# Optimization experiments

Measured on AMD Instinct MI355X. Metric: run time of the kernel, lower is better.

## Reference

```python
import jax, jax.numpy as jnp
import numpy as np

OFF_THRESH = 0.5  # specials.OFF_THRESH
INF = 1e10        # specials.INF


def _neighbor_gather(v):
    # v: [B, C, 3, 3, K, Hp, Wp] -> [B, C, 9, K, Hp, Wp]
    # entry (s,t) at output pixel (h,w) reads cell (s,t) of source pixel
    # (h-(s-1), w-(t-1)), i.e. the pixel whose window cell points at (h,w).
    B, C, _, _, K, Hp, Wp = v.shape
    vp = jnp.pad(v, ((0, 0), (0, 0), (0, 0), (0, 0), (0, 0), (1, 1), (1, 1)))
    slabs = [vp[:, :, s, t, :, 2 - s:2 - s + Hp, 2 - t:2 - t + Wp]
             for s in range(3) for t in range(3)]
    return jnp.stack(slabs, axis=2)


def _rays(cam_inv, Hp, Wp):
    # normalized (x/z, y/z) camera rays for padded pixel grid extended by 1
    xs = jnp.arange(-1, Wp + 1, dtype=jnp.float32)
    ys = jnp.arange(-1, Hp + 1, dtype=jnp.float32)
    u, v = jnp.meshgrid(xs, ys)                      # [Hp+2, Wp+2]
    hom = jnp.stack([u, v, jnp.ones_like(u)], 0)     # [3, Hp+2, Wp+2]
    r = jnp.einsum('ij,jhw->ihw', cam_inv, hom)
    return r[:2] / r[2:3]                            # [2, Hp+2, Wp+2]


def _smap_forward(x, cam):
    B = x.shape[0]
    H, W = x.shape[-2], x.shape[-1]
    Hp, Wp = H + 2, W + 2
    # add_pad: zero-pad spatially by 1 (3x3 window)
    xp = jnp.pad(x, ((0, 0), (0, 0), (1, 1), (1, 1)))
    xv, yv, zv, rm = xp[:, None, 0], xp[:, None, 1], xp[:, None, 2], xp[:, None, 3]  # [B,1,Hp,Wp]

    # ---- SMap3x3.forward ----
    cam_inv = jnp.linalg.inv(cam)
    rays = _rays(cam_inv, Hp, Wp)
    zs = jnp.where(zv > 0.0, zv, 1.0)
    px, py = xv / zs, yv / zs                        # projected normalized coords
    costs = []
    for s in range(3):
        for t in range(3):
            rx = rays[0, s:s + Hp, t:t + Wp]
            ry = rays[1, s:s + Hp, t:t + Wp]
            costs.append((px - rx) ** 2 + (py - ry) ** 2)
    key_query = jnp.stack(costs, axis=2)             # [B,1,9,Hp,Wp]

    idx = jnp.argmin(key_query, axis=2)              # argmax(-kq)
    weights_b = jax.nn.one_hot(idx, 9, axis=2, dtype=x.dtype)   # [B,1,9,Hp,Wp]
    valid = (rm > OFF_THRESH) & (zv > 0.0)           # [B,1,Hp,Wp]
    weights_b = jnp.where(valid[:, :, None], weights_b, 0.0)
    temp = jax.nn.one_hot(jnp.full((1,), 4), 9, dtype=x.dtype).reshape(1, 1, 9, 1, 1)
    bad = (rm > OFF_THRESH) & ~(zv > 0.0)
    weights_b = jnp.where(bad[:, :, None], temp, weights_b)

    xyz = jnp.stack([xv, yv, zv], axis=2)            # [B,1,3,Hp,Wp]
    wdet = jax.lax.stop_gradient(weights_b).reshape(B, 1, 3, 3, Hp, Wp)
    new_xyz = jnp.einsum('bcsthw,bczhw->bcstzhw', wdet, xyz)  # [B,1,3,3,3,Hp,Wp]
    weights_b2 = jnp.where(valid[:, :, None], weights_b, temp)
    new_rm = (jax.lax.stop_gradient(weights_b2) * rm[:, :, None]).reshape(B, 1, 3, 3, 1, Hp, Wp)
    nxz = jnp.concatenate([new_xyz, new_rm], axis=4)  # [B,1,3,3,4,Hp,Wp]

    # ---- calculate_weights ----
    zch = jax.lax.stop_gradient(nxz[:, :, :, :, 2:3])           # detached z channel
    gz = _neighbor_gather(zch)                                  # [B,1,9,1,Hp,Wp]
    gz = jnp.where(gz > 0.0, gz, INF)                           # agg(..., factor=INF)
    val = jnp.min(gz, axis=2, keepdims=True)
    sidx = jnp.argmin(gz, axis=2, keepdims=True)
    sidx = jnp.where((val > 0.0) & (val < INF), sidx, 4)
    sel = jax.nn.one_hot(sidx[:, :, 0], 9, axis=2, dtype=x.dtype)  # [B,1,9,1,Hp,Wp]
    gall = _neighbor_gather(nxz)                                # [B,1,9,4,Hp,Wp]
    out = jnp.sum(gall * sel, axis=2)                           # [B,1,4,Hp,Wp]
    # center crop back to original size
    out = out[:, :, :, 1:1 + H, 1:1 + W].reshape(B, 4, H, W)
    return out


def setup_inputs() -> dict:
    key = jax.random.key(0)
    k1, k2, k3 = jax.random.split(key, 3)
    B, H, W = 4, 512, 640
    xy = jax.random.normal(k1, (B, 2, H, W), dtype=jnp.float32)
    z = jax.random.uniform(k2, (B, 1, H, W), minval=0.5, maxval=5.0, dtype=jnp.float32)
    m = jax.random.uniform(k3, (B, 1, H, W), dtype=jnp.float32)
    x = jnp.concatenate([xy, z, m], axis=1)          # channels: x, y, z, mask
    cam = jnp.asarray(np.array([[500.0, 0.0, W / 2.0],
                                [0.0, 500.0, H / 2.0],
                                [0.0, 0.0, 1.0]], dtype=np.float32))
    return {"x": x, "cam": cam}


def reference(x, cam):
    return _smap_forward(x, cam)
```

## Files before the change

### kernel.cpp

```cpp
#include <hip/hip_runtime.h>

#define BT 32
#define HT (BT + 2)
#define PP (HT + 1)

__global__ __launch_bounds__(256) void smap_fused(
    const float* __restrict__ x, const float* __restrict__ cam,
    float* __restrict__ out, int B, int H, int W)
{
    __shared__ float2 szk[HT][PP];
    __shared__ float2 sxy[HT][PP];
    __shared__ float  srm[HT][PP];

    const int b  = blockIdx.z;
    const int h0 = blockIdx.y * BT;
    const int w0 = blockIdx.x * BT;
    const int tx = threadIdx.x;
    const int ty = threadIdx.y;
    const int tid = ty * 32 + tx;

    const float a00 = cam[0], a01 = cam[1], a02 = cam[2];
    const float a10 = cam[3], a11 = cam[4], a12 = cam[5];
    const float a20 = cam[6], a21 = cam[7], a22 = cam[8];
    const float m00 = a11 * a22 - a12 * a21;
    const float m01 = a10 * a22 - a12 * a20;
    const float m02 = a10 * a21 - a11 * a20;
    const float det = a00 * m00 - a01 * m01 + a02 * m02;
    const float i00 = m00 / det;
    const float i01 = (a02 * a21 - a01 * a22) / det;
    const float i02 = (a01 * a12 - a02 * a11) / det;
    const float i10 = (a12 * a20 - a10 * a22) / det;
    const float i11 = (a00 * a22 - a02 * a20) / det;
    const float i12 = (a02 * a10 - a00 * a12) / det;
    const float i20 = m02 / det;
    const float i21 = (a01 * a20 - a00 * a21) / det;
    const float i22 = (a00 * a11 - a01 * a10) / det;

    const bool fastcam = (i20 == 0.0f) && (i21 == 0.0f) && (i22 == 1.0f);
    const bool fastsep = fastcam &&
        (__float_as_uint(i01) == 0u) && (__float_as_uint(i10) == 0u);

    const size_t HW = (size_t)H * W;
    const float* xb = x + (size_t)b * 4 * HW;

    for (int item = tid; item < HT * HT; item += 256) {
        const int i = item / HT, j = item - i * HT;
        const int gh = h0 - 1 + i, gw = w0 - 1 + j;
        float xv = 0.f, yv = 0.f, zv = 0.f, rm = 0.f;
        if (gh >= 0 && gh < H && gw >= 0 && gw < W) {
            const size_t off = (size_t)gh * W + gw;
            xv = xb[off];
            yv = xb[HW + off];
            zv = xb[2 * HW + off];
            rm = xb[3 * HW + off];
        }
        const float zs = (zv > 0.f) ? zv : 1.0f;
        const float px = __fdiv_rn(xv, zs);
        const float py = __fdiv_rn(yv, zs);

        float best = __builtin_inff();
        int bi = 0;
        if (fastsep) {
            float f[3], g[3];
            #pragma unroll
            for (int t = 0; t < 3; ++t) {
                const float u  = (float)(gw + t);
                const float rx = __fadd_rn(__fmul_rn(i00, u), i02);
                const float dx = __fsub_rn(px, rx);
                f[t] = __fmul_rn(dx, dx);
            }
            #pragma unroll
            for (int s = 0; s < 3; ++s) {
                const float v  = (float)(gh + s);
                const float ry = __fadd_rn(__fmul_rn(i11, v), i12);
                const float dy = __fsub_rn(py, ry);
                g[s] = __fmul_rn(dy, dy);
            }
            #pragma unroll
            for (int n = 0; n < 9; ++n) {
                const float c = __fadd_rn(f[n % 3], g[n / 3]);
                if (c < best) { best = c; bi = n; }
            }
        } else {
            float A0[3], A1[3], B0[3], B1[3];
            #pragma unroll
            for (int t = 0; t < 3; ++t) {
                const float u = (float)(gw + t);
                A0[t] = __fmul_rn(i00, u);
                A1[t] = __fmul_rn(i10, u);
            }
            #pragma unroll
            for (int s = 0; s < 3; ++s) {
                const float v = (float)(gh + s);
                B0[s] = __fmul_rn(i01, v);
                B1[s] = __fmul_rn(i11, v);
            }
            #pragma unroll
            for (int n = 0; n < 9; ++n) {
                const int s = n / 3, t = n % 3;
                const float r0 = __fadd_rn(__fadd_rn(A0[t], B0[s]), i02);
                const float r1 = __fadd_rn(__fadd_rn(A1[t], B1[s]), i12);
                float rx, ry;
                if (fastcam) {
                    rx = r0; ry = r1;
                } else {
                    const float u = (float)(gw + t), v = (float)(gh + s);
                    const float r2 = __fadd_rn(__fadd_rn(__fmul_rn(i20, u), __fmul_rn(i21, v)), i22);
                    rx = __fdiv_rn(r0, r2);
                    ry = __fdiv_rn(r1, r2);
                }
                const float dx = __fsub_rn(px, rx);
                const float dy = __fsub_rn(py, ry);
                const float c  = __fadd_rn(__fmul_rn(dx, dx), __fmul_rn(dy, dy));
                if (c < best) { best = c; bi = n; }
            }
        }

        const bool validp = (rm > 0.5f) && (zv > 0.0f);
        const bool badp   = (rm > 0.5f) && !(zv > 0.0f);
        const int k = validp ? bi : (badp ? 4 : 9);
        szk[i][j] = make_float2(zv, __int_as_float(k));
        sxy[i][j] = make_float2(xv, yv);
        srm[i][j] = rm;
    }
    __syncthreads();

    const int rbase = 4 * ty;
    float2 rA[3], rB[3], rC[3];
    #pragma unroll
    for (int c = 0; c < 3; ++c) {
        rA[c] = szk[rbase][tx + c];
        rB[c] = szk[rbase + 1][tx + c];
    }

    #pragma unroll
    for (int q = 0; q < 4; ++q) {
        const int rq = rbase + q;
        #pragma unroll
        for (int c = 0; c < 3; ++c) rC[c] = szk[rq + 2][tx + c];

        float bz = 1e10f;
        int bli = rq + 1, blj = tx + 1;
        #pragma unroll
        for (int t = 0; t < 3; ++t) {
            const float z = rC[2 - t].x;
            const int   k = __float_as_int(rC[2 - t].y);
            const float cand = (k == t && z > 0.f) ? z : 1e10f;
            if (cand < bz) { bz = cand; bli = rq + 2; blj = tx + 2 - t; }
        }
        #pragma unroll
        for (int t = 0; t < 3; ++t) {
            const float z = rB[2 - t].x;
            const int   k = __float_as_int(rB[2 - t].y);
            const float cand = (k == 3 + t && z > 0.f) ? z : 1e10f;
            if (cand < bz) { bz = cand; bli = rq + 1; blj = tx + 2 - t; }
        }
        #pragma unroll
        for (int t = 0; t < 3; ++t) {
            const float z = rA[2 - t].x;
            const int   k = __float_as_int(rA[2 - t].y);
            const float cand = (k == 6 + t && z > 0.f) ? z : 1e10f;
            if (cand < bz) { bz = cand; bli = rq; blj = tx + 2 - t; }
        }
        const bool found = bz < 1e10f;

        const float2 vxy = sxy[bli][blj];
        const float  vrm = srm[bli][blj];

        float ox, oy, oz, orm;
        if (found) {
            ox = vxy.x; oy = vxy.y; oz = bz; orm = vrm;
        } else {
            const int   kc = __float_as_int(rB[1].y);
            const float zc = rB[1].x;
            const bool  k4 = (kc == 4);
            const bool  validp = (vrm > 0.5f) && (zc > 0.f);
            ox = k4 ? vxy.x : 0.f;
            oy = k4 ? vxy.y : 0.f;
            oz = k4 ? zc    : 0.f;
            orm = (k4 || !validp) ? vrm : 0.f;
        }

        const int h = h0 + rq, w = w0 + tx;
        const size_t obase = (size_t)b * 4 * HW + (size_t)h * W + w;
        __builtin_nontemporal_store(ox,  &out[obase]);
        __builtin_nontemporal_store(oy,  &out[obase + HW]);
        __builtin_nontemporal_store(oz,  &out[obase + 2 * HW]);
        __builtin_nontemporal_store(orm, &out[obase + 3 * HW]);

        #pragma unroll
        for (int c = 0; c < 3; ++c) { rA[c] = rB[c]; rB[c] = rC[c]; }
    }
}

extern "C" void kernel_launch(void* const* d_in, const int* in_sizes, int n_in,
                              void* d_out, int out_size, void* d_ws, size_t ws_size,
                              hipStream_t stream) {
    const float* x   = (const float*)d_in[0];
    const float* cam = (const float*)d_in[1];
    float* out = (float*)d_out;
    const int H = 512, W = 640;
    const int B = in_sizes[0] / (4 * H * W);
    dim3 block(32, 8);
    dim3 grid((W + BT - 1) / BT, (H + BT - 1) / BT, B);
    hipLaunchKernelGGL(smap_fused, grid, block, 0, stream, x, cam, out, B, H, W);
}
```

Before: 19.69 us.

## Vectorize halo tile loads with float4 and split shared memory into per-channel planes

The tile load now reads each halo row as aligned float4 quads per channel, with a scalar fallback at image edges, instead of scalar per-pixel loads. Shared storage becomes separate planar arrays for x, y, z, mask and the k code, padded so that quads store aligned. Issuing both load items per thread before processing them is meant to cut global load instruction count and overlap memory latency. In exchange the tile fetches extra columns (40 wide instead of 34) and uses more shared memory, which may lower occupancy.

```diff
diff --git a/kernel.cpp b/kernel.cpp
--- a/kernel.cpp
+++ b/kernel.cpp
@@ -1,16 +1,21 @@
 #include <hip/hip_runtime.h>
 
 #define BT 32
-#define HT (BT + 2)
-#define PP (HT + 1)
+#define HT 34
+#define RW 40
+#define KP 35
+#define NQ 10
+#define NITEM (HT * NQ)
 
 __global__ __launch_bounds__(256) void smap_fused(
     const float* __restrict__ x, const float* __restrict__ cam,
     float* __restrict__ out, int B, int H, int W)
 {
-    __shared__ float2 szk[HT][PP];
-    __shared__ float2 sxy[HT][PP];
-    __shared__ float  srm[HT][PP];
+    __shared__ float sxr[HT][RW];
+    __shared__ float syr[HT][RW];
+    __shared__ float szr[HT][RW];
+    __shared__ float srr[HT][RW];
+    __shared__ float skf[HT][KP];
 
     const int b  = blockIdx.z;
     const int h0 = blockIdx.y * BT;
@@ -43,21 +48,39 @@
     const size_t HW = (size_t)H * W;
     const float* xb = x + (size_t)b * 4 * HW;
 
-    for (int item = tid; item < HT * HT; item += 256) {
-        const int i = item / HT, j = item - i * HT;
-        const int gh = h0 - 1 + i, gw = w0 - 1 + j;
-        float xv = 0.f, yv = 0.f, zv = 0.f, rm = 0.f;
-        if (gh >= 0 && gh < H && gw >= 0 && gw < W) {
-            const size_t off = (size_t)gh * W + gw;
-            xv = xb[off];
-            yv = xb[HW + off];
-            zv = xb[2 * HW + off];
-            rm = xb[3 * HW + off];
-        }
+    auto ldq = [&](int row, int q, float4& X, float4& Y, float4& Z, float4& R) {
+        X = make_float4(0.f, 0.f, 0.f, 0.f); Y = X; Z = X; R = X;
+        const int gh = h0 - 1 + row;
+        const int gc = w0 - 4 + 4 * q;
+        if (gh >= 0 && gh < H) {
+            if (gc >= 0 && gc + 4 <= W) {
+                const size_t base = (size_t)gh * W + gc;
+                X = *(const float4*)(xb + base);
+                Y = *(const float4*)(xb + HW + base);
+                Z = *(const float4*)(xb + 2 * HW + base);
+                R = *(const float4*)(xb + 3 * HW + base);
+            } else {
+                float* Xa = (float*)&X; float* Ya = (float*)&Y;
+                float* Za = (float*)&Z; float* Ra = (float*)&R;
+                #pragma unroll
+                for (int e = 0; e < 4; ++e) {
+                    const int c = gc + e;
+                    if (c >= 0 && c < W) {
+                        const size_t off = (size_t)gh * W + c;
+                        Xa[e] = xb[off];
+                        Ya[e] = xb[HW + off];
+                        Za[e] = xb[2 * HW + off];
+                        Ra[e] = xb[3 * HW + off];
+                    }
+                }
+            }
+        }
+    };
+
+    auto kcode = [&](float xv, float yv, float zv, float rm, int gh, int gw) -> int {
         const float zs = (zv > 0.f) ? zv : 1.0f;
         const float px = __fdiv_rn(xv, zs);
         const float py = __fdiv_rn(yv, zs);
-
         float best = __builtin_inff();
         int bi = 0;
         if (fastsep) {
@@ -101,9 +124,8 @@
                 const float r0 = __fadd_rn(__fadd_rn(A0[t], B0[s]), i02);
                 const float r1 = __fadd_rn(__fadd_rn(A1[t], B1[s]), i12);
                 float rx, ry;
-                if (fastcam) {
-                    rx = r0; ry = r1;
-                } else {
+                if (fastcam) { rx = r0; ry = r1; }
+                else {
                     const float u = (float)(gw + t), v = (float)(gh + s);
                     const float r2 = __fadd_rn(__fadd_rn(__fmul_rn(i20, u), __fmul_rn(i21, v)), i22);
                     rx = __fdiv_rn(r0, r2);
@@ -115,69 +137,102 @@
                 if (c < best) { best = c; bi = n; }
             }
         }
-
         const bool validp = (rm > 0.5f) && (zv > 0.0f);
         const bool badp   = (rm > 0.5f) && !(zv > 0.0f);
-        const int k = validp ? bi : (badp ? 4 : 9);
-        szk[i][j] = make_float2(zv, __int_as_float(k));
-        sxy[i][j] = make_float2(xv, yv);
-        srm[i][j] = rm;
+        return validp ? bi : (badp ? 4 : 9);
+    };
+
+    auto proc = [&](int row, int q, const float4& X, const float4& Y,
+                    const float4& Z, const float4& R) {
+        *(float4*)&sxr[row][4 * q] = X;
+        *(float4*)&syr[row][4 * q] = Y;
+        *(float4*)&szr[row][4 * q] = Z;
+        *(float4*)&srr[row][4 * q] = R;
+        const int gh = h0 - 1 + row;
+        const float Xa[4] = {X.x, X.y, X.z, X.w};
+        const float Ya[4] = {Y.x, Y.y, Y.z, Y.w};
+        const float Za[4] = {Z.x, Z.y, Z.z, Z.w};
+        const float Ra[4] = {R.x, R.y, R.z, R.w};
+        #pragma unroll
+        for (int e = 0; e < 4; ++e) {
+            const int j = 4 * q + e - 3;
+            if (j < 0 || j >= HT) continue;
+            const int gw = w0 - 1 + j;
+            skf[row][j] = __int_as_float(kcode(Xa[e], Ya[e], Za[e], Ra[e], gh, gw));
+        }
+    };
+
+    {
+        const int item0 = tid;
+        const int item1 = tid + 256;
+        const bool act1 = item1 < NITEM;
+        const int row0 = item0 / NQ, q0 = item0 - row0 * NQ;
+        const int row1 = item1 / NQ, q1 = item1 - row1 * NQ;
+        float4 X0, Y0, Z0, R0, X1, Y1, Z1, R1;
+        ldq(row0, q0, X0, Y0, Z0, R0);
+        if (act1) ldq(row1, q1, X1, Y1, Z1, R1);
+        proc(row0, q0, X0, Y0, Z0, R0);
+        if (act1) proc(row1, q1, X1, Y1, Z1, R1);
     }
     __syncthreads();
 
     const int rbase = 4 * ty;
-    float2 rA[3], rB[3], rC[3];
+    float zA[3], zB[3], zC[3];
+    int   kA[3], kB[3], kC[3];
     #pragma unroll
     for (int c = 0; c < 3; ++c) {
-        rA[c] = szk[rbase][tx + c];
-        rB[c] = szk[rbase + 1][tx + c];
+        zA[c] = szr[rbase][tx + 3 + c];
+        kA[c] = __float_as_int(skf[rbase][tx + c]);
+        zB[c] = szr[rbase + 1][tx + 3 + c];
+        kB[c] = __float_as_int(skf[rbase + 1][tx + c]);
     }
 
     #pragma unroll
     for (int q = 0; q < 4; ++q) {
         const int rq = rbase + q;
         #pragma unroll
-        for (int c = 0; c < 3; ++c) rC[c] = szk[rq + 2][tx + c];
+        for (int c = 0; c < 3; ++c) {
+            zC[c] = szr[rq + 2][tx + 3 + c];
+            kC[c] = __float_as_int(skf[rq + 2][tx + c]);
+        }
 
         float bz = 1e10f;
         int bli = rq + 1, blj = tx + 1;
         #pragma unroll
         for (int t = 0; t < 3; ++t) {
-            const float z = rC[2 - t].x;
-            const int   k = __float_as_int(rC[2 - t].y);
-            const float cand = (k == t && z > 0.f) ? z : 1e10f;
+            const float z = zC[2 - t];
+            const float cand = (kC[2 - t] == t && z > 0.f) ? z : 1e10f;
             if (cand < bz) { bz = cand; bli = rq + 2; blj = tx + 2 - t; }
         }
         #pragma unroll
         for (int t = 0; t < 3; ++t) {
-            const float z = rB[2 - t].x;
-            const int   k = __float_as_int(rB[2 - t].y);
-            const float cand = (k == 3 + t && z > 0.f) ? z : 1e10f;
+            const float z = zB[2 - t];
+            const float cand = (kB[2 - t] == 3 + t && z > 0.f) ? z : 1e10f;
             if (cand < bz) { bz = cand; bli = rq + 1; blj = tx + 2 - t; }
         }
         #pragma unroll
         for (int t = 0; t < 3; ++t) {
-            const float z = rA[2 - t].x;
-            const int   k = __float_as_int(rA[2 - t].y);
-            const float cand = (k == 6 + t && z > 0.f) ? z : 1e10f;
+            const float z = zA[2 - t];
+            const float cand = (kA[2 - t] == 6 + t && z > 0.f) ? z : 1e10f;
             if (cand < bz) { bz = cand; bli = rq; blj = tx + 2 - t; }
         }
         const bool found = bz < 1e10f;
 
-        const float2 vxy = sxy[bli][blj];
-        const float  vrm = srm[bli][blj];
+        const float vx  = sxr[bli][blj + 3];
+        const float vy  = syr[bli][blj + 3];
+        const float vrm = srr[bli][blj + 3];
 
         float ox, oy, oz, orm;
         if (found) {
-            ox = vxy.x; oy = vxy.y; oz = bz; orm = vrm;
+            ox = vx; oy = vy; oz = bz; orm = vrm;
         } else {
-            const int   kc = __float_as_int(rB[1].y);
-            const float zc = rB[1].x;
+            const int   kc = kB[1];
+            const float zc = zB[1];
             const bool  k4 = (kc == 4);
             const bool  validp = (vrm > 0.5f) && (zc > 0.f);
-            ox = k4 ? vxy.x : 0.f;
-            oy = k4 ? vxy.y : 0.f;
-            oz = k4 ? zc    : 0.f;
+            ox = k4 ? vx : 0.f;
+            oy = k4 ? vy : 0.f;
+            oz = k4 ? zc : 0.f;
             orm = (k4 || !validp) ? vrm : 0.f;
         }
 
@@ -189,7 +244,10 @@
         __builtin_nontemporal_store(orm, &out[obase + 3 * HW]);
 
         #pragma unroll
-        for (int c = 0; c < 3; ++c) { rA[c] = rB[c]; rB[c] = rC[c]; }
+        for (int c = 0; c < 3; ++c) {
+            zA[c] = zB[c]; kA[c] = kB[c];
+            zB[c] = zC[c]; kB[c] = kC[c];
+        }
     }
 }
 
```

Result: slower. 20.91 us (+6.2%).

## Shrink tiles to 16x16, drop xy/rm shared arrays, remap blocks, outline generic path

Applied to the files above, without the earlier changes.

Tiles shrink from 32x32 to 16x16, with one output pixel per thread instead of four. The sxy and srm shared arrays are removed: the winning neighbour's x, y and mask are re-read from global memory, relying on cache hits. Block indices are swizzled across groups of eight, presumably to spread tiles across XCDs. The rarely used generic-camera path moves into a noinline function to cut register pressure, with launch bounds raised to 8 blocks per CU. The cost is a larger halo overhead per tile (18x18 for 16x16), extra global reads, and an assumption that H and W divide evenly by 16.

```diff
diff --git a/kernel.cpp b/kernel.cpp
--- a/kernel.cpp
+++ b/kernel.cpp
@@ -1,23 +1,70 @@
 #include <hip/hip_runtime.h>
 
-#define BT 32
-#define HT (BT + 2)
-#define PP (HT + 1)
-
-__global__ __launch_bounds__(256) void smap_fused(
+#define BT 16
+#define HT 18
+#define PP 19
+
+__device__ __attribute__((noinline))
+int kcode_generic(float px, float py, int gh, int gw,
+                  float i00, float i01, float i02,
+                  float i10, float i11, float i12,
+                  float i20, float i21, float i22, int fastcam)
+{
+    float A0[3], A1[3], B0[3], B1[3];
+    #pragma unroll
+    for (int t = 0; t < 3; ++t) {
+        const float u = (float)(gw + t);
+        A0[t] = __fmul_rn(i00, u);
+        A1[t] = __fmul_rn(i10, u);
+    }
+    #pragma unroll
+    for (int s = 0; s < 3; ++s) {
+        const float v = (float)(gh + s);
+        B0[s] = __fmul_rn(i01, v);
+        B1[s] = __fmul_rn(i11, v);
+    }
+    float best = __builtin_inff();
+    int bi = 0;
+    #pragma unroll
+    for (int n = 0; n < 9; ++n) {
+        const int s = n / 3, t = n % 3;
+        const float r0 = __fadd_rn(__fadd_rn(A0[t], B0[s]), i02);
+        const float r1 = __fadd_rn(__fadd_rn(A1[t], B1[s]), i12);
+        float rx, ry;
+        if (fastcam) { rx = r0; ry = r1; }
+        else {
+            const float u = (float)(gw + t), v = (float)(gh + s);
+            const float r2 = __fadd_rn(__fadd_rn(__fmul_rn(i20, u), __fmul_rn(i21, v)), i22);
+            rx = __fdiv_rn(r0, r2);
+            ry = __fdiv_rn(r1, r2);
+        }
+        const float dx = __fsub_rn(px, rx);
+        const float dy = __fsub_rn(py, ry);
+        const float c  = __fadd_rn(__fmul_rn(dx, dx), __fmul_rn(dy, dy));
+        if (c < best) { best = c; bi = n; }
+    }
+    return bi;
+}
+
+__global__ __launch_bounds__(256, 8) void smap_fused(
     const float* __restrict__ x, const float* __restrict__ cam,
     float* __restrict__ out, int B, int H, int W)
 {
     __shared__ float2 szk[HT][PP];
-    __shared__ float2 sxy[HT][PP];
-    __shared__ float  srm[HT][PP];
-
-    const int b  = blockIdx.z;
-    const int h0 = blockIdx.y * BT;
-    const int w0 = blockIdx.x * BT;
+
+    const int tiles_x = W / BT, tiles_y = H / BT;
+    const int ntiles = tiles_x * tiles_y * B;
+    int bid = blockIdx.x + tiles_x * (blockIdx.y + tiles_y * blockIdx.z);
+    if ((ntiles & 7) == 0) bid = (bid & 7) * (ntiles >> 3) + (bid >> 3);
+    const int txt = bid % tiles_x;
+    const int rest = bid / tiles_x;
+    const int tyt = rest % tiles_y;
+    const int b   = rest / tiles_y;
+
+    const int h0 = tyt * BT, w0 = txt * BT;
     const int tx = threadIdx.x;
     const int ty = threadIdx.y;
-    const int tid = ty * 32 + tx;
+    const int tid = ty * 16 + tx;
 
     const float a00 = cam[0], a01 = cam[1], a02 = cam[2];
     const float a10 = cam[3], a11 = cam[4], a12 = cam[5];
@@ -58,8 +105,7 @@
         const float px = __fdiv_rn(xv, zs);
         const float py = __fdiv_rn(yv, zs);
 
-        float best = __builtin_inff();
-        int bi = 0;
+        int bi;
         if (fastsep) {
             float f[3], g[3];
             #pragma unroll
@@ -76,121 +122,83 @@
                 const float dy = __fsub_rn(py, ry);
                 g[s] = __fmul_rn(dy, dy);
             }
+            float best = __builtin_inff();
+            bi = 0;
             #pragma unroll
             for (int n = 0; n < 9; ++n) {
                 const float c = __fadd_rn(f[n % 3], g[n / 3]);
                 if (c < best) { best = c; bi = n; }
             }
         } else {
-            float A0[3], A1[3], B0[3], B1[3];
-            #pragma unroll
-            for (int t = 0; t < 3; ++t) {
-                const float u = (float)(gw + t);
-                A0[t] = __fmul_rn(i00, u);
-                A1[t] = __fmul_rn(i10, u);
-            }
-            #pragma unroll
-            for (int s = 0; s < 3; ++s) {
-                const float v = (float)(gh + s);
-                B0[s] = __fmul_rn(i01, v);
-                B1[s] = __fmul_rn(i11, v);
-            }
-            #pragma unroll
-            for (int n = 0; n < 9; ++n) {
-                const int s = n / 3, t = n % 3;
-                const float r0 = __fadd_rn(__fadd_rn(A0[t], B0[s]), i02);
-                const float r1 = __fadd_rn(__fadd_rn(A1[t], B1[s]), i12);
-                float rx, ry;
-                if (fastcam) {
-                    rx = r0; ry = r1;
-                } else {
-                    const float u = (float)(gw + t), v = (float)(gh + s);
-                    const float r2 = __fadd_rn(__fadd_rn(__fmul_rn(i20, u), __fmul_rn(i21, v)), i22);
-                    rx = __fdiv_rn(r0, r2);
-                    ry = __fdiv_rn(r1, r2);
-                }
-                const float dx = __fsub_rn(px, rx);
-                const float dy = __fsub_rn(py, ry);
-                const float c  = __fadd_rn(__fmul_rn(dx, dx), __fmul_rn(dy, dy));
-                if (c < best) { best = c; bi = n; }
-            }
+            bi = kcode_generic(px, py, gh, gw, i00, i01, i02,
+                               i10, i11, i12, i20, i21, i22, (int)fastcam);
         }
 
         const bool validp = (rm > 0.5f) && (zv > 0.0f);
         const bool badp   = (rm > 0.5f) && !(zv > 0.0f);
         const int k = validp ? bi : (badp ? 4 : 9);
         szk[i][j] = make_float2(zv, __int_as_float(k));
-        sxy[i][j] = make_float2(xv, yv);
-        srm[i][j] = rm;
     }
     __syncthreads();
 
-    const int rbase = 4 * ty;
-    float2 rA[3], rB[3], rC[3];
+    float2 cA[3], cB[3], cC[3];
     #pragma unroll
     for (int c = 0; c < 3; ++c) {
-        rA[c] = szk[rbase][tx + c];
-        rB[c] = szk[rbase + 1][tx + c];
-    }
-
-    #pragma unroll
-    for (int q = 0; q < 4; ++q) {
-        const int rq = rbase + q;
-        #pragma unroll
-        for (int c = 0; c < 3; ++c) rC[c] = szk[rq + 2][tx + c];
-
-        float bz = 1e10f;
-        int bli = rq + 1, blj = tx + 1;
-        #pragma unroll
-        for (int t = 0; t < 3; ++t) {
-            const float z = rC[2 - t].x;
-            const int   k = __float_as_int(rC[2 - t].y);
-            const float cand = (k == t && z > 0.f) ? z : 1e10f;
-            if (cand < bz) { bz = cand; bli = rq + 2; blj = tx + 2 - t; }
-        }
-        #pragma unroll
-        for (int t = 0; t < 3; ++t) {
-            const float z = rB[2 - t].x;
-            const int   k = __float_as_int(rB[2 - t].y);
-            const float cand = (k == 3 + t && z > 0.f) ? z : 1e10f;
-            if (cand < bz) { bz = cand; bli = rq + 1; blj = tx + 2 - t; }
-        }
-        #pragma unroll
-        for (int t = 0; t < 3; ++t) {
-            const float z = rA[2 - t].x;
-            const int   k = __float_as_int(rA[2 - t].y);
-            const float cand = (k == 6 + t && z > 0.f) ? z : 1e10f;
-            if (cand < bz) { bz = cand; bli = rq; blj = tx + 2 - t; }
-        }
-        const bool found = bz < 1e10f;
-
-        const float2 vxy = sxy[bli][blj];
-        const float  vrm = srm[bli][blj];
-
-        float ox, oy, oz, orm;
-        if (found) {
-            ox = vxy.x; oy = vxy.y; oz = bz; orm = vrm;
-        } else {
-            const int   kc = __float_as_int(rB[1].y);
-            const float zc = rB[1].x;
-            const bool  k4 = (kc == 4);
-            const bool  validp = (vrm > 0.5f) && (zc > 0.f);
-            ox = k4 ? vxy.x : 0.f;
-            oy = k4 ? vxy.y : 0.f;
-            oz = k4 ? zc    : 0.f;
-            orm = (k4 || !validp) ? vrm : 0.f;
-        }
-
-        const int h = h0 + rq, w = w0 + tx;
-        const size_t obase = (size_t)b * 4 * HW + (size_t)h * W + w;
-        __builtin_nontemporal_store(ox,  &out[obase]);
-        __builtin_nontemporal_store(oy,  &out[obase + HW]);
-        __builtin_nontemporal_store(oz,  &out[obase + 2 * HW]);
-        __builtin_nontemporal_store(orm, &out[obase + 3 * HW]);
-
-        #pragma unroll
-        for (int c = 0; c < 3; ++c) { rA[c] = rB[c]; rB[c] = rC[c]; }
-    }
+        cA[c] = szk[ty][tx + c];
+        cB[c] = szk[ty + 1][tx + c];
+        cC[c] = szk[ty + 2][tx + c];
+    }
+
+    float bz = 1e10f;
+    int bli = ty + 1, blj = tx + 1;
+    #pragma unroll
+    for (int t = 0; t < 3; ++t) {
+        const float z = cC[2 - t].x;
+        const int   k = __float_as_int(cC[2 - t].y);
+        const float cand = (k == t && z > 0.f) ? z : 1e10f;
+        if (cand < bz) { bz = cand; bli = ty + 2; blj = tx + 2 - t; }
+    }
+    #pragma unroll
+    for (int t = 0; t < 3; ++t) {
+        const float z = cB[2 - t].x;
+        const int   k = __float_as_int(cB[2 - t].y);
+        const float cand = (k == 3 + t && z > 0.f) ? z : 1e10f;
+        if (cand < bz) { bz = cand; bli = ty + 1; blj = tx + 2 - t; }
+    }
+    #pragma unroll
+    for (int t = 0; t < 3; ++t) {
+        const float z = cA[2 - t].x;
+        const int   k = __float_as_int(cA[2 - t].y);
+        const float cand = (k == 6 + t && z > 0.f) ? z : 1e10f;
+        if (cand < bz) { bz = cand; bli = ty; blj = tx + 2 - t; }
+    }
+    const bool found = bz < 1e10f;
+
+    const size_t woff = (size_t)(h0 - 1 + bli) * W + (w0 - 1 + blj);
+    const float vx  = xb[woff];
+    const float vy  = xb[HW + woff];
+    const float vrm = xb[3 * HW + woff];
+
+    float ox, oy, oz, orm;
+    if (found) {
+        ox = vx; oy = vy; oz = bz; orm = vrm;
+    } else {
+        const int   kc = __float_as_int(cB[1].y);
+        const float zc = cB[1].x;
+        const bool  k4 = (kc == 4);
+        const bool  validp = (vrm > 0.5f) && (zc > 0.f);
+        ox = k4 ? vx : 0.f;
+        oy = k4 ? vy : 0.f;
+        oz = k4 ? zc : 0.f;
+        orm = (k4 || !validp) ? vrm : 0.f;
+    }
+
+    const int h = h0 + ty, w = w0 + tx;
+    const size_t obase = (size_t)b * 4 * HW + (size_t)h * W + w;
+    __builtin_nontemporal_store(ox,  &out[obase]);
+    __builtin_nontemporal_store(oy,  &out[obase + HW]);
+    __builtin_nontemporal_store(oz,  &out[obase + 2 * HW]);
+    __builtin_nontemporal_store(orm, &out[obase + 3 * HW]);
 }
 
 extern "C" void kernel_launch(void* const* d_in, const int* in_sizes, int n_in,
@@ -201,7 +209,7 @@
     float* out = (float*)d_out;
     const int H = 512, W = 640;
     const int B = in_sizes[0] / (4 * H * W);
-    dim3 block(32, 8);
-    dim3 grid((W + BT - 1) / BT, (H + BT - 1) / BT, B);
+    dim3 block(16, 16);
+    dim3 grid(W / BT, H / BT, B);
     hipLaunchKernelGGL(smap_fused, grid, block, 0, stream, x, cam, out, B, H, W);
 }
```

Measured after the change: 20.44 us. +3.8%, slower.
